# Optimization experiments

Measured on AMD Instinct MI355X. Metric: run time of the kernel, lower is better.

Reference implementation:

```python
import jax, jax.numpy as jnp
import numpy as np

D_K = 128
SCALER = np.sqrt(D_K).astype(np.float32)

def setup_inputs() -> dict:
    key = jax.random.key(0)
    kq, kk, kv = jax.random.split(key, 3)
    B, L, D = 16, 2048, D_K
    q = jax.random.normal(kq, (B, L, D), dtype=jnp.float32)
    k = jax.random.normal(kk, (B, L, D), dtype=jnp.float32)
    v = jax.random.normal(kv, (B, L, D), dtype=jnp.float32)
    return {"q": q, "k": k, "v": v}

def reference(q, k, v):
    # score[b, i, j] = q[b, i, :] . k[b, j, :] / sqrt(d_k)
    score = jnp.einsum('bid,bjd->bij', q, k) / SCALER
    attn = jax.nn.softmax(score, axis=-1)
    # output[b, i, :] = sum_j attn[b, i, j] * v[b, j, :]
    return jnp.einsum('bij,bjd->bid', attn, v)
```

## Files before the change

### kernel.cpp

```cpp
#include <hip/hip_runtime.h>
#include <stdint.h>


typedef short bf16x8 __attribute__((ext_vector_type(8)));
typedef float f32x4 __attribute__((ext_vector_type(4)));

#define L_SEQ  2048
#define D_HEAD 128
#define TKV    64
#define NIT    (L_SEQ / TKV)
#define KST    136
#define VST    72
#define PST    72
#define OST    132

#define K_OFF  0
#define V_OFF  17408
#define P_OFF  (17408 + 18432)
#define SMEM_BYTES (P_OFF + 4*32*PST*2)

__device__ __forceinline__ unsigned pk2(float lo, float hi) {
    union { float f; unsigned u; } a, b;
    a.f = lo; b.f = hi;
    return __builtin_amdgcn_perm(b.u + 0x8000u, a.u + 0x8000u, 0x07060302u);
}
__device__ __forceinline__ float ex2(float x) { return __builtin_amdgcn_exp2f(x); }

union F4 { float4 v; float f[4]; };

__global__ __launch_bounds__(256, 1)
void attn_fwd(const float* __restrict__ Qg, const float* __restrict__ Kg,
              const float* __restrict__ Vg, float* __restrict__ Og) {
    __shared__ __align__(16) char smem[SMEM_BYTES];
    unsigned short* Kl = (unsigned short*)(smem + K_OFF);
    unsigned short* Vl = (unsigned short*)(smem + V_OFF);
    float*          Ol = (float*)smem;

    const int tid  = threadIdx.x;
    const int wv   = tid >> 6;
    const int lane = tid & 63;
    const int c    = lane & 15;
    const int qd   = lane >> 4;
    unsigned short* Pl = (unsigned short*)(smem + P_OFF) + wv * (32 * PST);

    const int b  = blockIdx.x & 15;
    const int qb = blockIdx.x >> 4;

    const float* Qb = Qg + (size_t)b * L_SEQ * D_HEAD;
    const float* Kb = Kg + (size_t)b * L_SEQ * D_HEAD;
    const float* Vb = Vg + (size_t)b * L_SEQ * D_HEAD;

    const int krow = tid >> 2, kch = tid & 3;
    const int vcc  = tid & 31, vgk = tid >> 5;

    const float QS = 1.4426950408889634f / 11.313708498984761f;
    bf16x8 qf[2][4];
    #pragma unroll
    for (int s = 0; s < 2; ++s) {
        const float* qrow = Qb + (size_t)(qb * 128 + wv * 32 + s * 16 + c) * D_HEAD + qd * 8;
        #pragma unroll
        for (int kt = 0; kt < 4; ++kt) {
            float4 x0 = *(const float4*)(qrow + kt * 32);
            float4 x1 = *(const float4*)(qrow + kt * 32 + 4);
            union { unsigned u[4]; bf16x8 v; } t;
            t.u[0] = pk2(x0.x * QS, x0.y * QS);
            t.u[1] = pk2(x0.z * QS, x0.w * QS);
            t.u[2] = pk2(x1.x * QS, x1.y * QS);
            t.u[3] = pk2(x1.z * QS, x1.w * QS);
            qf[s][kt] = t.v;
        }
    }

    F4 kreg[8], vreg[8];
    {
        const float* kp = Kb + (size_t)krow * D_HEAD + kch * 32;
        #pragma unroll
        for (int r = 0; r < 8; ++r) kreg[r].v = *(const float4*)(kp + r * 4);
        const float* vp = Vb + (size_t)(vgk * 8) * D_HEAD + vcc * 4;
        #pragma unroll
        for (int r = 0; r < 8; ++r) vreg[r].v = *(const float4*)(vp + (size_t)r * D_HEAD);
    }

    f32x4 acc[2][8];
    #pragma unroll
    for (int s = 0; s < 2; ++s)
        #pragma unroll
        for (int dt = 0; dt < 8; ++dt) acc[s][dt] = (f32x4){0.f, 0.f, 0.f, 0.f};
    float lrun[2] = {0.f, 0.f};

    for (int it = 0; it < NIT; ++it) {
        #pragma unroll
        for (int i = 0; i < 4; ++i) {
            uint4 w;
            w.x = pk2(kreg[2*i].f[0],   kreg[2*i].f[1]);
            w.y = pk2(kreg[2*i].f[2],   kreg[2*i].f[3]);
            w.z = pk2(kreg[2*i+1].f[0], kreg[2*i+1].f[1]);
            w.w = pk2(kreg[2*i+1].f[2], kreg[2*i+1].f[3]);
            *(uint4*)(&Kl[krow * KST + kch * 32 + i * 8]) = w;
        }
        #pragma unroll
        for (int dd = 0; dd < 4; ++dd) {
            uint4 w;
            w.x = pk2(vreg[0].f[dd], vreg[1].f[dd]);
            w.y = pk2(vreg[2].f[dd], vreg[3].f[dd]);
            w.z = pk2(vreg[4].f[dd], vreg[5].f[dd]);
            w.w = pk2(vreg[6].f[dd], vreg[7].f[dd]);
            *(uint4*)(&Vl[(vcc * 4 + dd) * VST + vgk * 8]) = w;
        }
        __syncthreads();

        if (it + 1 < NIT) {
            const float* kp = Kb + (size_t)((it + 1) * TKV + krow) * D_HEAD + kch * 32;
            #pragma unroll
            for (int r = 0; r < 8; ++r) kreg[r].v = *(const float4*)(kp + r * 4);
            const float* vp = Vb + (size_t)((it + 1) * TKV + vgk * 8) * D_HEAD + vcc * 4;
            #pragma unroll
            for (int r = 0; r < 8; ++r) vreg[r].v = *(const float4*)(vp + (size_t)r * D_HEAD);
        }

        f32x4 st[4][2];
        #pragma unroll
        for (int v = 0; v < 4; ++v) { st[v][0] = (f32x4){0,0,0,0}; st[v][1] = (f32x4){0,0,0,0}; }
        #pragma unroll
        for (int kt = 0; kt < 4; ++kt) {
            #pragma unroll
            for (int v = 0; v < 4; ++v) {
                bf16x8 a = *(const bf16x8*)(&Kl[(v * 16 + c) * KST + kt * 32 + qd * 8]);
                st[v][0] = __builtin_amdgcn_mfma_f32_16x16x32_bf16(a, qf[0][kt], st[v][0], 0, 0, 0);
                st[v][1] = __builtin_amdgcn_mfma_f32_16x16x32_bf16(a, qf[1][kt], st[v][1], 0, 0, 0);
            }
        }

        #pragma unroll
        for (int s = 0; s < 2; ++s) {
            float lsum = 0.f;
            #pragma unroll
            for (int v = 0; v < 4; ++v) {
                float p0 = ex2(st[v][s].x), p1 = ex2(st[v][s].y);
                float p2 = ex2(st[v][s].z), p3 = ex2(st[v][s].w);
                lsum += (p0 + p1) + (p2 + p3);
                uint2 w; w.x = pk2(p0, p1); w.y = pk2(p2, p3);
                *(uint2*)(&Pl[(s * 16 + c) * PST + v * 16 + qd * 4]) = w;
            }
            lrun[s] += lsum;
        }
        bf16x8 pf[2][2];
        #pragma unroll
        for (int h = 0; h < 2; ++h)
            #pragma unroll
            for (int s = 0; s < 2; ++s)
                pf[h][s] = *(const bf16x8*)(&Pl[(s * 16 + c) * PST + h * 32 + qd * 8]);

        #pragma unroll
        for (int dt = 0; dt < 8; ++dt) {
            #pragma unroll
            for (int h = 0; h < 2; ++h) {
                bf16x8 a = *(const bf16x8*)(&Vl[(dt * 16 + c) * VST + h * 32 + qd * 8]);
                acc[0][dt] = __builtin_amdgcn_mfma_f32_16x16x32_bf16(a, pf[h][0], acc[0][dt], 0, 0, 0);
                acc[1][dt] = __builtin_amdgcn_mfma_f32_16x16x32_bf16(a, pf[h][1], acc[1][dt], 0, 0, 0);
            }
        }
        __syncthreads();
    }

    float inv[2];
    #pragma unroll
    for (int s = 0; s < 2; ++s) {
        float l = lrun[s];
        l += __shfl_xor(l, 16);
        l += __shfl_xor(l, 32);
        inv[s] = 1.0f / l;
    }
    #pragma unroll
    for (int pass = 0; pass < 2; ++pass) {
        if ((wv >> 1) == pass) {
            int rw = (wv & 1) * 32;
            #pragma unroll
            for (int s = 0; s < 2; ++s)
                #pragma unroll
                for (int dt = 0; dt < 8; ++dt) {
                    f32x4 o = acc[s][dt];
                    float4 w = {o.x * inv[s], o.y * inv[s], o.z * inv[s], o.w * inv[s]};
                    *(float4*)(&Ol[(rw + s * 16 + c) * OST + dt * 16 + qd * 4]) = w;
                }
        }
        __syncthreads();
        #pragma unroll
        for (int i = 0; i < 8; ++i) {
            int idx = i * 256 + tid;
            int row = idx >> 5, c4 = idx & 31;
            float4 val = *(const float4*)(&Ol[row * OST + c4 * 4]);
            size_t q = (size_t)b * L_SEQ + qb * 128 + pass * 64 + row;
            *(float4*)(Og + q * D_HEAD + c4 * 4) = val;
        }
        __syncthreads();
    }
}

extern "C" void kernel_launch(void* const* d_in, const int* in_sizes, int n_in,
                              void* d_out, int out_size, void* d_ws, size_t ws_size,
                              hipStream_t stream) {
    const float* q = (const float*)d_in[0];
    const float* k = (const float*)d_in[1];
    const float* v = (const float*)d_in[2];
    float* out = (float*)d_out;
    dim3 grid(256), block(256);
    attn_fwd<<<grid, block, 0, stream>>>(q, k, v, out);
}
```

Baseline: 166.3 us.

## Split attention into bf16 K/V prepass, split-KV attention, and combine kernels

Adds a prepass kernel that converts K and V to bf16 once, storing K with an XOR-swizzled layout and V transposed and swizzled into workspace. The main attention kernel splits the KV sequence three ways across 768 blocks to fill more CUs, loads tiles directly into LDS with global_load_lds, and uses swizzled LDS indexing in place of padding. A combine kernel sums the three bf16 partial outputs and normalizes them with the summed row sums. This removes the per-block redundant fp32-to-bf16 conversion of K/V and the low occupancy of 256 blocks, at the cost of extra launches, workspace traffic and bf16 rounding of the partial outputs.

```diff
diff --git a/kernel.cpp b/kernel.cpp
--- a/kernel.cpp
+++ b/kernel.cpp
@@ -4,20 +4,15 @@
 
 typedef short bf16x8 __attribute__((ext_vector_type(8)));
 typedef float f32x4 __attribute__((ext_vector_type(4)));
+typedef unsigned int u32;
+typedef unsigned short u16;
 
 #define L_SEQ  2048
 #define D_HEAD 128
-#define TKV    64
-#define NIT    (L_SEQ / TKV)
-#define KST    136
-#define VST    72
-#define PST    72
-#define OST    132
-
-#define K_OFF  0
-#define V_OFF  17408
-#define P_OFF  (17408 + 18432)
-#define SMEM_BYTES (P_OFF + 4*32*PST*2)
+#define TSZ    8388608u
+#define W_PART (2u * TSZ)
+#define W_LSUM (W_PART + 768u * 32768u)
+#define WS_NEED (W_LSUM + 768u * 128u * 4u)
 
 __device__ __forceinline__ unsigned pk2(float lo, float hi) {
     union { float f; unsigned u; } a, b;
@@ -25,60 +20,113 @@
     return __builtin_amdgcn_perm(b.u + 0x8000u, a.u + 0x8000u, 0x07060302u);
 }
 __device__ __forceinline__ float ex2(float x) { return __builtin_amdgcn_exp2f(x); }
-
-union F4 { float4 v; float f[4]; };
-
-__global__ __launch_bounds__(256, 1)
-void attn_fwd(const float* __restrict__ Qg, const float* __restrict__ Kg,
-              const float* __restrict__ Vg, float* __restrict__ Og) {
-    __shared__ __align__(16) char smem[SMEM_BYTES];
-    unsigned short* Kl = (unsigned short*)(smem + K_OFF);
-    unsigned short* Vl = (unsigned short*)(smem + V_OFF);
-    float*          Ol = (float*)smem;
-
-    const int tid  = threadIdx.x;
-    const int wv   = tid >> 6;
-    const int lane = tid & 63;
-    const int c    = lane & 15;
-    const int qd   = lane >> 4;
-    unsigned short* Pl = (unsigned short*)(smem + P_OFF) + wv * (32 * PST);
-
-    const int b  = blockIdx.x & 15;
-    const int qb = blockIdx.x >> 4;
-
-    const float* Qb = Qg + (size_t)b * L_SEQ * D_HEAD;
-    const float* Kb = Kg + (size_t)b * L_SEQ * D_HEAD;
-    const float* Vb = Vg + (size_t)b * L_SEQ * D_HEAD;
-
-    const int krow = tid >> 2, kch = tid & 3;
-    const int vcc  = tid & 31, vgk = tid >> 5;
+__device__ __forceinline__ float bflo(unsigned w) {
+    union { unsigned u; float f; } v; v.u = w << 16; return v.f;
+}
+__device__ __forceinline__ float bfhi(unsigned w) {
+    union { unsigned u; float f; } v; v.u = w & 0xffff0000u; return v.f;
+}
+__device__ __forceinline__ void gl_lds16(const u16* g, u16* l) {
+    __builtin_amdgcn_global_load_lds(
+        (const __attribute__((address_space(1))) u32*)g,
+        (__attribute__((address_space(3))) u32*)l, 16, 0, 0);
+}
+
+__global__ __launch_bounds__(256, 4)
+void prepass(const float* __restrict__ K, const float* __restrict__ V,
+             u16* __restrict__ kb, u16* __restrict__ vt) {
+    const int id = blockIdx.x, t = threadIdx.x;
+    if (id < 512) {
+        const float* src = K + (size_t)id * 64 * 128;
+        u16*        dst = kb + (size_t)id * 64 * 128;
+        const int r = t >> 2;
+        #pragma unroll
+        for (int i = 0; i < 4; ++i) {
+            int gp = (t & 3) * 4 + i;
+            int gs = gp ^ (r & 7);
+            const float* s = src + r * 128 + gs * 8;
+            float4 x0 = *(const float4*)s, x1 = *(const float4*)(s + 4);
+            uint4 w;
+            w.x = pk2(x0.x, x0.y); w.y = pk2(x0.z, x0.w);
+            w.z = pk2(x1.x, x1.y); w.w = pk2(x1.z, x1.w);
+            *(uint4*)(dst + r * 128 + gp * 8) = w;
+        }
+    } else {
+        __shared__ __align__(16) u16 vl[128 * 72];
+        const int bid = id - 512;
+        const float* src = V + (size_t)bid * 64 * 128;
+        const int vcc = t & 31, vgk = t >> 5;
+        union { float4 v; float f[4]; } vr[8];
+        const float* vp = src + (size_t)(vgk * 8) * 128 + vcc * 4;
+        #pragma unroll
+        for (int r = 0; r < 8; ++r) vr[r].v = *(const float4*)(vp + (size_t)r * 128);
+        #pragma unroll
+        for (int dd = 0; dd < 4; ++dd) {
+            uint4 w;
+            w.x = pk2(vr[0].f[dd], vr[1].f[dd]);
+            w.y = pk2(vr[2].f[dd], vr[3].f[dd]);
+            w.z = pk2(vr[4].f[dd], vr[5].f[dd]);
+            w.w = pk2(vr[6].f[dd], vr[7].f[dd]);
+            *(uint4*)(&vl[(vcc * 4 + dd) * 72 + vgk * 8]) = w;
+        }
+        __syncthreads();
+        u16* dst = vt + (size_t)bid * 8192;
+        #pragma unroll
+        for (int i = 0; i < 4; ++i) {
+            int flat = t + 256 * i;
+            int d = flat >> 3, gp = flat & 7;
+            uint4 w = *(const uint4*)(&vl[d * 72 + ((gp ^ (d & 7)) * 8)]);
+            *(uint4*)(dst + (size_t)flat * 8) = w;
+        }
+    }
+}
+
+__global__ __launch_bounds__(256, 2)
+void attn3(const float* __restrict__ Qg, const u16* __restrict__ kb,
+           const u16* __restrict__ vt, u16* __restrict__ part,
+           float* __restrict__ lsum) {
+    __shared__ __align__(16) char smem[49152];
+    const int tid = threadIdx.x;
+    const int wv = tid >> 6, lane = tid & 63;
+    const int c = lane & 15, qd = lane >> 4, cx = c & 7;
+    const int bid = blockIdx.x;
+    const int p = bid & 255, kvh = bid >> 8;
+    const int b = p & 15, qblk = p >> 4;
+    const int t0 = kvh * 11;
+    const int nt = (kvh < 2) ? 11 : 10;
+
+    const float* Qp = Qg + (size_t)b * L_SEQ * D_HEAD;
+    const u16*   Kp = kb + (size_t)b * L_SEQ * D_HEAD + (size_t)t0 * 8192;
+    const u16*   Vp = vt + (size_t)b * 32 * 8192 + (size_t)t0 * 8192;
+    u16* Kl = (u16*)smem;
+    u16* Vl = (u16*)(smem + 16384);
+    u16* Pl = (u16*)(smem + 32768) + wv * 2048;
+
+    const int so = wv * 2048 + lane * 8;
+    const int psw = (c & 7) << 1;
+
+    #pragma unroll
+    for (int i = 0; i < 4; ++i) {
+        gl_lds16(Kp + so + i * 512, Kl + so + i * 512);
+        gl_lds16(Vp + so + i * 512, Vl + so + i * 512);
+    }
 
     const float QS = 1.4426950408889634f / 11.313708498984761f;
     bf16x8 qf[2][4];
     #pragma unroll
     for (int s = 0; s < 2; ++s) {
-        const float* qrow = Qb + (size_t)(qb * 128 + wv * 32 + s * 16 + c) * D_HEAD + qd * 8;
+        const float* qrow = Qp + (size_t)(qblk * 128 + wv * 32 + s * 16 + c) * 128 + qd * 8;
         #pragma unroll
         for (int kt = 0; kt < 4; ++kt) {
             float4 x0 = *(const float4*)(qrow + kt * 32);
             float4 x1 = *(const float4*)(qrow + kt * 32 + 4);
-            union { unsigned u[4]; bf16x8 v; } t;
-            t.u[0] = pk2(x0.x * QS, x0.y * QS);
-            t.u[1] = pk2(x0.z * QS, x0.w * QS);
-            t.u[2] = pk2(x1.x * QS, x1.y * QS);
-            t.u[3] = pk2(x1.z * QS, x1.w * QS);
-            qf[s][kt] = t.v;
-        }
-    }
-
-    F4 kreg[8], vreg[8];
-    {
-        const float* kp = Kb + (size_t)krow * D_HEAD + kch * 32;
-        #pragma unroll
-        for (int r = 0; r < 8; ++r) kreg[r].v = *(const float4*)(kp + r * 4);
-        const float* vp = Vb + (size_t)(vgk * 8) * D_HEAD + vcc * 4;
-        #pragma unroll
-        for (int r = 0; r < 8; ++r) vreg[r].v = *(const float4*)(vp + (size_t)r * D_HEAD);
+            union { unsigned u[4]; bf16x8 v; } tt;
+            tt.u[0] = pk2(x0.x * QS, x0.y * QS);
+            tt.u[1] = pk2(x0.z * QS, x0.w * QS);
+            tt.u[2] = pk2(x1.x * QS, x1.y * QS);
+            tt.u[3] = pk2(x1.z * QS, x1.w * QS);
+            qf[s][kt] = tt.v;
+        }
     }
 
     f32x4 acc[2][8];
@@ -88,109 +136,142 @@
         for (int dt = 0; dt < 8; ++dt) acc[s][dt] = (f32x4){0.f, 0.f, 0.f, 0.f};
     float lrun[2] = {0.f, 0.f};
 
-    for (int it = 0; it < NIT; ++it) {
-        #pragma unroll
-        for (int i = 0; i < 4; ++i) {
-            uint4 w;
-            w.x = pk2(kreg[2*i].f[0],   kreg[2*i].f[1]);
-            w.y = pk2(kreg[2*i].f[2],   kreg[2*i].f[3]);
-            w.z = pk2(kreg[2*i+1].f[0], kreg[2*i+1].f[1]);
-            w.w = pk2(kreg[2*i+1].f[2], kreg[2*i+1].f[3]);
-            *(uint4*)(&Kl[krow * KST + kch * 32 + i * 8]) = w;
-        }
-        #pragma unroll
-        for (int dd = 0; dd < 4; ++dd) {
-            uint4 w;
-            w.x = pk2(vreg[0].f[dd], vreg[1].f[dd]);
-            w.y = pk2(vreg[2].f[dd], vreg[3].f[dd]);
-            w.z = pk2(vreg[4].f[dd], vreg[5].f[dd]);
-            w.w = pk2(vreg[6].f[dd], vreg[7].f[dd]);
-            *(uint4*)(&Vl[(vcc * 4 + dd) * VST + vgk * 8]) = w;
-        }
-        __syncthreads();
-
-        if (it + 1 < NIT) {
-            const float* kp = Kb + (size_t)((it + 1) * TKV + krow) * D_HEAD + kch * 32;
-            #pragma unroll
-            for (int r = 0; r < 8; ++r) kreg[r].v = *(const float4*)(kp + r * 4);
-            const float* vp = Vb + (size_t)((it + 1) * TKV + vgk * 8) * D_HEAD + vcc * 4;
-            #pragma unroll
-            for (int r = 0; r < 8; ++r) vreg[r].v = *(const float4*)(vp + (size_t)r * D_HEAD);
-        }
-
+    __syncthreads();
+
+    for (int it = 0; it < nt; ++it) {
         f32x4 st[4][2];
         #pragma unroll
-        for (int v = 0; v < 4; ++v) { st[v][0] = (f32x4){0,0,0,0}; st[v][1] = (f32x4){0,0,0,0}; }
+        for (int v = 0; v < 4; ++v) {
+            st[v][0] = (f32x4){0.f, 0.f, 0.f, 0.f};
+            st[v][1] = (f32x4){0.f, 0.f, 0.f, 0.f};
+        }
         #pragma unroll
         for (int kt = 0; kt < 4; ++kt) {
+            const int g = ((kt * 4 + qd) ^ cx) * 8;
             #pragma unroll
             for (int v = 0; v < 4; ++v) {
-                bf16x8 a = *(const bf16x8*)(&Kl[(v * 16 + c) * KST + kt * 32 + qd * 8]);
+                bf16x8 a = *(const bf16x8*)(Kl + (v * 16 + c) * 128 + g);
                 st[v][0] = __builtin_amdgcn_mfma_f32_16x16x32_bf16(a, qf[0][kt], st[v][0], 0, 0, 0);
                 st[v][1] = __builtin_amdgcn_mfma_f32_16x16x32_bf16(a, qf[1][kt], st[v][1], 0, 0, 0);
             }
         }
+        __syncthreads();
+
+        if (it + 1 < nt) {
+            const u16* kg = Kp + (size_t)(it + 1) * 8192 + so;
+            #pragma unroll
+            for (int i = 0; i < 4; ++i) gl_lds16(kg + i * 512, Kl + so + i * 512);
+        }
 
         #pragma unroll
         for (int s = 0; s < 2; ++s) {
-            float lsum = 0.f;
+            float lsm = 0.f;
             #pragma unroll
             for (int v = 0; v < 4; ++v) {
                 float p0 = ex2(st[v][s].x), p1 = ex2(st[v][s].y);
                 float p2 = ex2(st[v][s].z), p3 = ex2(st[v][s].w);
-                lsum += (p0 + p1) + (p2 + p3);
+                lsm += (p0 + p1) + (p2 + p3);
                 uint2 w; w.x = pk2(p0, p1); w.y = pk2(p2, p3);
-                *(uint2*)(&Pl[(s * 16 + c) * PST + v * 16 + qd * 4]) = w;
+                int gsw = (v * 4 + qd) ^ psw;
+                *(uint2*)(Pl + (s * 16 + c) * 64 + gsw * 4) = w;
             }
-            lrun[s] += lsum;
+            lrun[s] += lsm;
         }
         bf16x8 pf[2][2];
         #pragma unroll
-        for (int h = 0; h < 2; ++h)
+        for (int h = 0; h < 2; ++h) {
+            int gsw = (h * 8 + qd * 2) ^ psw;
             #pragma unroll
             for (int s = 0; s < 2; ++s)
-                pf[h][s] = *(const bf16x8*)(&Pl[(s * 16 + c) * PST + h * 32 + qd * 8]);
+                pf[h][s] = *(const bf16x8*)(Pl + (s * 16 + c) * 64 + gsw * 4);
+        }
 
         #pragma unroll
         for (int dt = 0; dt < 8; ++dt) {
             #pragma unroll
             for (int h = 0; h < 2; ++h) {
-                bf16x8 a = *(const bf16x8*)(&Vl[(dt * 16 + c) * VST + h * 32 + qd * 8]);
+                bf16x8 a = *(const bf16x8*)(Vl + (dt * 16 + c) * 64 + ((h * 4 + qd) ^ cx) * 8);
                 acc[0][dt] = __builtin_amdgcn_mfma_f32_16x16x32_bf16(a, pf[h][0], acc[0][dt], 0, 0, 0);
                 acc[1][dt] = __builtin_amdgcn_mfma_f32_16x16x32_bf16(a, pf[h][1], acc[1][dt], 0, 0, 0);
             }
         }
         __syncthreads();
-    }
-
-    float inv[2];
+
+        if (it + 1 < nt) {
+            const u16* vg = Vp + (size_t)(it + 1) * 8192 + so;
+            #pragma unroll
+            for (int i = 0; i < 4; ++i) gl_lds16(vg + i * 512, Vl + so + i * 512);
+        }
+    }
+
+    float ls[2];
     #pragma unroll
     for (int s = 0; s < 2; ++s) {
         float l = lrun[s];
         l += __shfl_xor(l, 16);
         l += __shfl_xor(l, 32);
-        inv[s] = 1.0f / l;
-    }
-    #pragma unroll
-    for (int pass = 0; pass < 2; ++pass) {
-        if ((wv >> 1) == pass) {
-            int rw = (wv & 1) * 32;
-            #pragma unroll
-            for (int s = 0; s < 2; ++s)
-                #pragma unroll
-                for (int dt = 0; dt < 8; ++dt) {
-                    f32x4 o = acc[s][dt];
-                    float4 w = {o.x * inv[s], o.y * inv[s], o.z * inv[s], o.w * inv[s]};
-                    *(float4*)(&Ol[(rw + s * 16 + c) * OST + dt * 16 + qd * 4]) = w;
-                }
-        }
-        __syncthreads();
+        ls[s] = l;
+    }
+    u16* pb = part + (size_t)bid * 16384;
+    #pragma unroll
+    for (int s = 0; s < 2; ++s)
+        #pragma unroll
+        for (int dt = 0; dt < 8; ++dt) {
+            f32x4 o = acc[s][dt];
+            uint2 w; w.x = pk2(o.x, o.y); w.y = pk2(o.z, o.w);
+            *(uint2*)(pb + ((((wv * 2 + s) * 8 + dt) * 64 + lane) << 2)) = w;
+        }
+    if (qd == 0) {
+        lsum[kvh * 32768 + p * 128 + wv * 32 + c]      = ls[0];
+        lsum[kvh * 32768 + p * 128 + wv * 32 + 16 + c] = ls[1];
+    }
+}
+
+__global__ __launch_bounds__(256, 2)
+void combine3(const u16* __restrict__ part, const float* __restrict__ lsum,
+              float* __restrict__ Og) {
+    __shared__ float inv[128];
+    __shared__ __align__(16) float Ol[64 * 132];
+    const int t = threadIdx.x, p = blockIdx.x;
+    const int b = p & 15, qblk = p >> 4;
+    if (t < 128) {
+        float l0 = lsum[p * 128 + t];
+        float l1 = lsum[32768 + p * 128 + t];
+        float l2 = lsum[65536 + p * 128 + t];
+        inv[t] = 1.0f / (l0 + l1 + l2);
+    }
+    const uint2* P0 = (const uint2*)(part + (size_t)p * 16384);
+    const uint2* P1 = (const uint2*)(part + (size_t)(256 + p) * 16384);
+    const uint2* P2 = (const uint2*)(part + (size_t)(512 + p) * 16384);
+    __syncthreads();
+    #pragma unroll
+    for (int h = 0; h < 2; ++h) {
         #pragma unroll
         for (int i = 0; i < 8; ++i) {
-            int idx = i * 256 + tid;
-            int row = idx >> 5, c4 = idx & 31;
-            float4 val = *(const float4*)(&Ol[row * OST + c4 * 4]);
-            size_t q = (size_t)b * L_SEQ + qb * 128 + pass * 64 + row;
+            int slot = i * 256 + t;
+            int lc = slot >> 6, lane = slot & 63;
+            int gc = h * 32 + lc;
+            int s = (lc >> 3) & 1, dt = lc & 7;
+            int qd = lane >> 4, c = lane & 15;
+            int row = (lc >> 4) * 32 + s * 16 + c;
+            int d0 = dt * 16 + qd * 4;
+            size_t idx = (size_t)gc * 64 + lane;
+            uint2 w0 = P0[idx], w1 = P1[idx], w2 = P2[idx];
+            float iv = inv[h * 64 + row];
+            float4 o;
+            o.x = (bflo(w0.x) + bflo(w1.x) + bflo(w2.x)) * iv;
+            o.y = (bfhi(w0.x) + bfhi(w1.x) + bfhi(w2.x)) * iv;
+            o.z = (bflo(w0.y) + bflo(w1.y) + bflo(w2.y)) * iv;
+            o.w = (bfhi(w0.y) + bfhi(w1.y) + bfhi(w2.y)) * iv;
+            *(float4*)(&Ol[row * 132 + d0]) = o;
+        }
+        __syncthreads();
+        #pragma unroll
+        for (int i = 0; i < 8; ++i) {
+            int slot = i * 256 + t;
+            int row = slot >> 5, c4 = slot & 31;
+            float4 val = *(const float4*)(&Ol[row * 132 + c4 * 4]);
+            size_t q = (size_t)b * L_SEQ + qblk * 128 + h * 64 + row;
             *(float4*)(Og + q * D_HEAD + c4 * 4) = val;
         }
         __syncthreads();
@@ -204,6 +285,11 @@
     const float* k = (const float*)d_in[1];
     const float* v = (const float*)d_in[2];
     float* out = (float*)d_out;
-    dim3 grid(256), block(256);
-    attn_fwd<<<grid, block, 0, stream>>>(q, k, v, out);
-}
+    u16* kb = (u16*)d_ws;
+    u16* vt = (u16*)((char*)d_ws + TSZ);
+    u16* part = (u16*)((char*)d_ws + W_PART);
+    float* ls = (float*)((char*)d_ws + W_LSUM);
+    prepass<<<dim3(1024), dim3(256), 0, stream>>>(k, v, kb, vt);
+    attn3<<<dim3(768), dim3(256), 0, stream>>>(q, kb, vt, part, ls);
+    combine3<<<dim3(256), dim3(256), 0, stream>>>(part, ls, out);
+}
```

Result: faster. 139.9 us (-15.9%).
